# Kernel tuning notes

Measured on AMD Instinct MI355X. Metric: run time of the kernel, lower is better.

Reference implementation:

```python
import jax, jax.numpy as jnp
import numpy as np

B, N, D, H = 8, 2048, 768, 64

def setup_inputs() -> dict:
    key = jax.random.key(0)
    k1, k2, k3, k4 = jax.random.split(key, 4)
    return {
        "input": jax.random.normal(k1, (B, N, D), dtype=jnp.float32),
        "Wq": jax.random.normal(k2, (D, H), dtype=jnp.float32) * (D ** -0.5),
        "Wk": jax.random.normal(k3, (D, H), dtype=jnp.float32) * (D ** -0.5),
        "Wv": jax.random.normal(k4, (D, H), dtype=jnp.float32) * (D ** -0.5),
    }

def reference(input, Wq, Wk, Wv):
    # Projections: [B, N, H]
    Q = jnp.einsum('bnd,dh->bnh', input, Wq)
    K = jnp.einsum('bnd,dh->bnh', input, Wk)
    V = jnp.einsum('bnd,dh->bnh', input, Wv)
    # Raw scores [B, N, N]; mask BEFORE scaling (as in original; -inf/scale == -inf)
    scores = jnp.einsum('bqh,bkh->bqk', Q, K)
    n = input.shape[1]
    causal = jnp.tril(jnp.ones((n, n), dtype=bool))
    scores = jnp.where(causal, scores, -jnp.inf)
    scores = scores / (K.shape[-1] ** 0.5)
    attn = jax.nn.softmax(scores, axis=-1)
    # dropout_rate=0 -> identity (eval mode)
    return jnp.einsum('bqk,bkh->bqh', attn, V)
```

## Files before the change

### kernel.cpp

```cpp
#include <hip/hip_runtime.h>
#include <stdint.h>

typedef __bf16 bf16_t;
typedef __bf16 bf16x8 __attribute__((ext_vector_type(8)));
typedef float floatx4 __attribute__((ext_vector_type(4)));
typedef float floatx16 __attribute__((ext_vector_type(16)));

#define B_ 8
#define N_ 2048
#define D_ 768
#define H_ 64

#define WAIT_VM0()   { __builtin_amdgcn_sched_barrier(0); __builtin_amdgcn_s_waitcnt(0x0F70); __builtin_amdgcn_sched_barrier(0); }
#define WAIT_LGKM0() { __builtin_amdgcn_sched_barrier(0); __builtin_amdgcn_s_waitcnt(0xC07F); __builtin_amdgcn_sched_barrier(0); }

__device__ __forceinline__ bf16_t f2bf(float f) {
    return (bf16_t)f;
}

__device__ __forceinline__ uint32_t pkbf(float lo, float hi_) {
    union { bf16_t b[2]; uint32_t u; } t;
    t.b[0] = (bf16_t)lo; t.b[1] = (bf16_t)hi_;
    return t.u;
}

__device__ __forceinline__ void async_cp16(void* l, const void* g) {
    __builtin_amdgcn_global_load_lds(
        (const __attribute__((address_space(1))) uint32_t*)g,
        (__attribute__((address_space(3))) uint32_t*)l, 16, 0, 0);
}

__global__ void wt_kernel(const float* __restrict__ Wq,
                          const float* __restrict__ Wk,
                          const float* __restrict__ Wv,
                          bf16_t* __restrict__ Wt) {
    const int h = threadIdx.x;
    const int k = blockIdx.x;
    const int s = blockIdx.y;
    const float* W = (s == 0) ? Wq : (s == 1) ? Wk : Wv;
    float v = W[k * H_ + h];
    if (s == 0) v *= 0.125f * 1.4426950408889634f;
    Wt[(size_t)(s * 64 + h) * D_ + k] = f2bf(v);
}

__launch_bounds__(512, 4)
__global__ void proj_kernel(const float* __restrict__ X,
                            const bf16_t* __restrict__ Wt,
                            bf16_t* __restrict__ Qb,
                            bf16_t* __restrict__ Kb,
                            bf16_t* __restrict__ Vt) {
    const int wave = threadIdx.x >> 6;
    const int lane = threadIdx.x & 63;
    const int quad = lane >> 4;
    const int l16  = lane & 15;
    const int rowhalf = wave >> 2;
    const int colq    = wave & 3;
    const int m0blk = blockIdx.x * 32;

    __shared__ __align__(16) float  As[2][32 * 64];
    __shared__ __align__(16) bf16_t Bs[2][192 * 64];

    floatx4 acc[3];
#pragma unroll
    for (int i = 0; i < 3; i++) acc[i] = (floatx4){0.f, 0.f, 0.f, 0.f};

    auto stage = [&](int buf, int k0) {
        {
            const int r = wave * 4 + (lane >> 4);
            const int c = (lane & 15) ^ (r & 15);
            const float* g = X + (size_t)(m0blk + r) * D_ + k0 + c * 4;
            async_cp16((char*)&As[buf][0] + wave * 1024, g);
        }
#pragma unroll
        for (int i = 0; i < 3; i++) {
            const int r = (wave * 3 + i) * 8 + (lane >> 3);
            const int c = (lane & 7) ^ (r & 7);
            const bf16_t* g = Wt + (size_t)r * D_ + k0 + c * 8;
            async_cp16((char*)&Bs[buf][0] + (wave * 3 + i) * 1024, g);
        }
    };

    const int arow = rowhalf * 16 + l16;

    stage(0, 0);
    for (int ch = 0; ch < 12; ch++) {
        __syncthreads();
        if (ch + 1 < 12) stage((ch + 1) & 1, (ch + 1) * 64);

        const char* Ab = (const char*)&As[ch & 1][0];
        const char* Bb = (const char*)&Bs[ch & 1][0];
#pragma unroll
        for (int kh = 0; kh < 2; kh++) {
            const int c0 = kh * 8 + quad * 2;
            float4 xa = *(const float4*)(Ab + arow * 256 + ((c0 ^ l16) & 15) * 16);
            float4 xb = *(const float4*)(Ab + arow * 256 + (((c0 + 1) ^ l16) & 15) * 16);
            bf16x8 af;
            af[0] = f2bf(xa.x); af[1] = f2bf(xa.y);
            af[2] = f2bf(xa.z); af[3] = f2bf(xa.w);
            af[4] = f2bf(xb.x); af[5] = f2bf(xb.y);
            af[6] = f2bf(xb.z); af[7] = f2bf(xb.w);
            const int cb = kh * 4 + quad;
#pragma unroll
            for (int nt = 0; nt < 3; nt++) {
                const int nl = colq * 48 + nt * 16 + l16;
                bf16x8 bf = *(const bf16x8*)(Bb + nl * 128 + ((cb ^ (nl & 7))) * 16);
                acc[nt] = __builtin_amdgcn_mfma_f32_16x16x32_bf16(af, bf, acc[nt], 0, 0, 0);
            }
        }
    }

#pragma unroll
    for (int nt = 0; nt < 3; nt++) {
        const int c = colq * 48 + nt * 16 + l16;
#pragma unroll
        for (int r = 0; r < 4; r++) {
            const int m = m0blk + rowhalf * 16 + quad * 4 + r;
            bf16_t val = f2bf(acc[nt][r]);
            if (c < 64) {
                Qb[(size_t)m * H_ + c] = val;
            } else if (c < 128) {
                Kb[(size_t)m * H_ + (c - 64)] = val;
            } else {
                const int b = m >> 11, n = m & 2047, h = c - 128;
                Vt[((size_t)b * H_ + h) * N_ + n] = val;
            }
        }
    }
}

__launch_bounds__(512, 4)
__global__ void attn_kernel(const bf16_t* __restrict__ Qb,
                            const bf16_t* __restrict__ Kb,
                            const bf16_t* __restrict__ Vt,
                            float* __restrict__ Out) {
    const int x = blockIdx.x;
    const int b = blockIdx.y;
    const int z = blockIdx.z;
    const int qt = z ? (63 - x) : x;
    const int q0 = qt * 32;

    const int tid  = threadIdx.x;
    const int wave = tid >> 6;
    const int lane = tid & 63;
    const int hi   = lane >> 5;
    const int lq   = lane & 31;

    __shared__ __align__(16) char smem[8 * 8192 + 1024];
    char* mybase = smem + wave * 8192;
    float* Ol = (float*)smem;
    float* Ll = (float*)(smem + 65536);

    const bf16_t* KpB = Kb + (size_t)b * N_ * H_;
    const bf16_t* VpB = Vt + (size_t)b * H_ * N_;

    const bf16_t* qrow = Qb + ((size_t)b * N_ + q0 + lq) * H_ + hi * 8;
    bf16x8 qf0 = *(const bf16x8*)(qrow);
    bf16x8 qf1 = *(const bf16x8*)(qrow + 16);
    bf16x8 qf2 = *(const bf16x8*)(qrow + 32);
    bf16x8 qf3 = *(const bf16x8*)(qrow + 48);

    floatx16 o0, o1;
#pragma unroll
    for (int i = 0; i < 16; i++) { o0[i] = 0.f; o1[i] = 0.f; }
    float ls = 0.f;

    const int rK = lane >> 3, cK = lane & 7;
    auto stage_k = [&](int k0, char* buf) {
#pragma unroll
        for (int i = 0; i < 4; i++) {
            const int r = i * 8 + rK;
            const int mk = rK ^ ((i & 1) << 2);
            async_cp16(buf + i * 1024,
                       KpB + (size_t)(k0 + r) * H_ + (cK ^ mk) * 8);
        }
    };

    const int ktm = qt;
    if (wave <= ktm)     stage_k(wave * 32, mybase);
    if (wave + 8 <= ktm) stage_k((wave + 8) * 32, mybase + 4096);

    const int mK = (lq & 7) ^ ((lq & 8) >> 1);

    for (int kt = wave; kt <= ktm; kt += 8) {
        const int k0 = kt * 32;
        char* kb = mybase + (((kt - wave) >> 3) & 1) * 4096;

        if (kt == wave) { WAIT_VM0(); }

        bf16x8 kf0 = *(const bf16x8*)(kb + lq * 128 + (((0 + hi) ^ mK) * 16));
        bf16x8 kf1 = *(const bf16x8*)(kb + lq * 128 + (((2 + hi) ^ mK) * 16));
        bf16x8 kf2 = *(const bf16x8*)(kb + lq * 128 + (((4 + hi) ^ mK) * 16));
        bf16x8 kf3 = *(const bf16x8*)(kb + lq * 128 + (((6 + hi) ^ mK) * 16));
        WAIT_LGKM0();

        const bf16_t* vrow0 = VpB + (size_t)lq * N_ + k0 + 8 * hi;
        const bf16_t* vrow1 = vrow0 + (size_t)32 * N_;
        bf16x8 vf00 = *(const bf16x8*)(vrow0);
        bf16x8 vf01 = *(const bf16x8*)(vrow0 + 16);
        bf16x8 vf10 = *(const bf16x8*)(vrow1);
        bf16x8 vf11 = *(const bf16x8*)(vrow1 + 16);
        __builtin_amdgcn_sched_barrier(0);
        if (kt + 16 <= ktm) stage_k(k0 + 512, kb);

        floatx16 st;
#pragma unroll
        for (int i = 0; i < 16; i++) st[i] = 0.f;
        st = __builtin_amdgcn_mfma_f32_32x32x16_bf16(kf0, qf0, st, 0, 0, 0);
        st = __builtin_amdgcn_mfma_f32_32x32x16_bf16(kf1, qf1, st, 0, 0, 0);
        st = __builtin_amdgcn_mfma_f32_32x32x16_bf16(kf2, qf2, st, 0, 0, 0);
        st = __builtin_amdgcn_mfma_f32_32x32x16_bf16(kf3, qf3, st, 0, 0, 0);

        if (kt < qt) {
#pragma unroll
            for (int r = 0; r < 16; r++) st[r] = exp2f(st[r]);
        } else {
#pragma unroll
            for (int r = 0; r < 16; r++) {
                const int row = (r & 3) + 8 * (r >> 2) + 4 * hi;
                st[r] = (row <= lq) ? exp2f(st[r]) : 0.f;
            }
        }
        {
            float t0 = (st[0] + st[1]) + (st[2] + st[3]);
            float t1 = (st[4] + st[5]) + (st[6] + st[7]);
            float t2 = (st[8] + st[9]) + (st[10] + st[11]);
            float t3 = (st[12] + st[13]) + (st[14] + st[15]);
            ls += (t0 + t1) + (t2 + t3);
        }

        uint32_t pb[8];
#pragma unroll
        for (int t = 0; t < 8; t++) pb[t] = pkbf(st[2 * t], st[2 * t + 1]);
        uint32_t rc[4];
#pragma unroll
        for (int t = 0; t < 4; t++) {
            const uint32_t w = hi ? pb[(t & 1) + 4 * (t >> 1)]
                                  : pb[(t & 1) + 2 + 4 * (t >> 1)];
            rc[t] = (uint32_t)__shfl_xor((int)w, 32, 64);
        }
        union { uint32_t u[4]; bf16x8 v; } f0, f1;
        f0.u[0] = hi ? rc[0] : pb[0]; f0.u[1] = hi ? rc[1] : pb[1];
        f0.u[2] = hi ? pb[2] : rc[0]; f0.u[3] = hi ? pb[3] : rc[1];
        f1.u[0] = hi ? rc[2] : pb[4]; f1.u[1] = hi ? rc[3] : pb[5];
        f1.u[2] = hi ? pb[6] : rc[2]; f1.u[3] = hi ? pb[7] : rc[3];

        o0 = __builtin_amdgcn_mfma_f32_32x32x16_bf16(f0.v, vf00, o0, 0, 0, 0);
        o0 = __builtin_amdgcn_mfma_f32_32x32x16_bf16(f1.v, vf01, o0, 0, 0, 0);
        o1 = __builtin_amdgcn_mfma_f32_32x32x16_bf16(f0.v, vf10, o1, 0, 0, 0);
        o1 = __builtin_amdgcn_mfma_f32_32x32x16_bf16(f1.v, vf11, o1, 0, 0, 0);
    }

    float lst = ls + __shfl_xor(ls, 32, 64);
    __syncthreads();
    if (hi == 0) Ll[wave * 32 + lq] = lst;
#pragma unroll
    for (int r = 0; r < 16; r++) {
        const int q = (r & 3) + 8 * (r >> 2) + 4 * hi;
        Ol[((size_t)wave * 32 + q) * 64 + lq]      = o0[r];
        Ol[((size_t)wave * 32 + q) * 64 + 32 + lq] = o1[r];
    }
    __syncthreads();
    {
        const int q  = tid >> 4;
        const int h4 = (tid & 15) * 4;
        floatx4 a = (floatx4){0.f, 0.f, 0.f, 0.f};
        float l = 0.f;
#pragma unroll
        for (int w = 0; w < 8; w++) {
            const floatx4 part = *(const floatx4*)&Ol[((size_t)w * 32 + q) * 64 + h4];
            a += part;
            l += Ll[w * 32 + q];
        }
        const float inv = 1.0f / l;
        float4 outv = {a[0] * inv, a[1] * inv, a[2] * inv, a[3] * inv};
        *(float4*)&Out[((size_t)b * N_ + q0 + q) * H_ + h4] = outv;
    }
}

extern "C" void kernel_launch(void* const* d_in, const int* in_sizes, int n_in,
                              void* d_out, int out_size, void* d_ws, size_t ws_size,
                              hipStream_t stream) {
    const float* X  = (const float*)d_in[0];
    const float* Wq = (const float*)d_in[1];
    const float* Wk = (const float*)d_in[2];
    const float* Wv = (const float*)d_in[3];
    float* Out = (float*)d_out;

    char* ws = (char*)d_ws;
    bf16_t* Qb = (bf16_t*)(ws);
    bf16_t* Kb = (bf16_t*)(ws + (size_t)(2u << 20));
    bf16_t* Vt = (bf16_t*)(ws + (size_t)(4u << 20));
    bf16_t* Wt = (bf16_t*)(ws + (size_t)(6u << 20));

    hipLaunchKernelGGL(wt_kernel, dim3(768, 3), dim3(64), 0, stream, Wq, Wk, Wv, Wt);
    hipLaunchKernelGGL(proj_kernel, dim3(512), dim3(512), 0, stream, X, Wt, Qb, Kb, Vt);
    hipLaunchKernelGGL(attn_kernel, dim3(32, 8, 2), dim3(512), 0, stream, Qb, Kb, Vt, Out);
}
```

Before: 113.9 us.

## Tile weight transpose via LDS, relax first K wait, use permlane32 swap

The weight-transpose kernel now transposes 64x64 tiles through shared memory with vectorized float4 loads and 16-byte bf16 stores, replacing strided scalar writes. The attention kernel's first wait only drains the first K tile when a second tile is in flight, leaving the prefetch outstanding. The cross-half exchange of probability fragments uses v_permlane32_swap instead of four shuffles plus selects. The wait count assumes exactly four loads per stage, and the swap asm depends on gfx950 support.

```diff
diff --git a/kernel.cpp b/kernel.cpp
--- a/kernel.cpp
+++ b/kernel.cpp
@@ -12,6 +12,7 @@
 #define H_ 64
 
 #define WAIT_VM0()   { __builtin_amdgcn_sched_barrier(0); __builtin_amdgcn_s_waitcnt(0x0F70); __builtin_amdgcn_sched_barrier(0); }
+#define WAIT_VM4()   { __builtin_amdgcn_sched_barrier(0); __builtin_amdgcn_s_waitcnt(0x0F74); __builtin_amdgcn_sched_barrier(0); }
 #define WAIT_LGKM0() { __builtin_amdgcn_sched_barrier(0); __builtin_amdgcn_s_waitcnt(0xC07F); __builtin_amdgcn_sched_barrier(0); }
 
 __device__ __forceinline__ bf16_t f2bf(float f) {
@@ -34,13 +35,34 @@
                           const float* __restrict__ Wk,
                           const float* __restrict__ Wv,
                           bf16_t* __restrict__ Wt) {
-    const int h = threadIdx.x;
-    const int k = blockIdx.x;
-    const int s = blockIdx.y;
+    const int kt = blockIdx.x;
+    const int s  = blockIdx.y;
     const float* W = (s == 0) ? Wq : (s == 1) ? Wk : Wv;
-    float v = W[k * H_ + h];
-    if (s == 0) v *= 0.125f * 1.4426950408889634f;
-    Wt[(size_t)(s * 64 + h) * D_ + k] = f2bf(v);
+    const float scale = (s == 0) ? 0.125f * 1.4426950408889634f : 1.0f;
+
+    __shared__ float T[64][65];
+    const int tid = threadIdx.x;
+    const int r  = tid >> 2;
+    const int cg = tid & 3;
+
+    const float4* src = (const float4*)(W + (size_t)(kt * 64 + r) * H_ + cg * 16);
+#pragma unroll
+    for (int j = 0; j < 4; j++) {
+        float4 v = src[j];
+        T[cg * 16 + j * 4 + 0][r] = v.x;
+        T[cg * 16 + j * 4 + 1][r] = v.y;
+        T[cg * 16 + j * 4 + 2][r] = v.z;
+        T[cg * 16 + j * 4 + 3][r] = v.w;
+    }
+    __syncthreads();
+
+    const int h = r;
+    bf16_t* dst = Wt + (size_t)(s * 64 + h) * D_ + kt * 64 + cg * 16;
+    union { bf16_t b[16]; uint4 q[2]; } o;
+#pragma unroll
+    for (int j = 0; j < 16; j++) o.b[j] = f2bf(T[h][cg * 16 + j] * scale);
+    ((uint4*)dst)[0] = o.q[0];
+    ((uint4*)dst)[1] = o.q[1];
 }
 
 __launch_bounds__(512, 4)
@@ -176,8 +198,9 @@
     };
 
     const int ktm = qt;
-    if (wave <= ktm)     stage_k(wave * 32, mybase);
-    if (wave + 8 <= ktm) stage_k((wave + 8) * 32, mybase + 4096);
+    const bool dbl = (wave + 8 <= ktm);
+    if (wave <= ktm) stage_k(wave * 32, mybase);
+    if (dbl)         stage_k((wave + 8) * 32, mybase + 4096);
 
     const int mK = (lq & 7) ^ ((lq & 8) >> 1);
 
@@ -185,7 +208,10 @@
         const int k0 = kt * 32;
         char* kb = mybase + (((kt - wave) >> 3) & 1) * 4096;
 
-        if (kt == wave) { WAIT_VM0(); }
+        if (kt == wave) {
+            if (dbl) { WAIT_VM4(); }
+            else     { WAIT_VM0(); }
+        }
 
         bf16x8 kf0 = *(const bf16x8*)(kb + lq * 128 + (((0 + hi) ^ mK) * 16));
         bf16x8 kf1 = *(const bf16x8*)(kb + lq * 128 + (((2 + hi) ^ mK) * 16));
@@ -231,18 +257,17 @@
         uint32_t pb[8];
 #pragma unroll
         for (int t = 0; t < 8; t++) pb[t] = pkbf(st[2 * t], st[2 * t + 1]);
-        uint32_t rc[4];
-#pragma unroll
-        for (int t = 0; t < 4; t++) {
-            const uint32_t w = hi ? pb[(t & 1) + 4 * (t >> 1)]
-                                  : pb[(t & 1) + 2 + 4 * (t >> 1)];
-            rc[t] = (uint32_t)__shfl_xor((int)w, 32, 64);
-        }
+        uint32_t a0 = pb[0], b0 = pb[2];
+        uint32_t a1 = pb[1], b1 = pb[3];
+        uint32_t a2 = pb[4], b2 = pb[6];
+        uint32_t a3 = pb[5], b3 = pb[7];
+        asm volatile("v_permlane32_swap_b32 %0, %1" : "+v"(a0), "+v"(b0));
+        asm volatile("v_permlane32_swap_b32 %0, %1" : "+v"(a1), "+v"(b1));
+        asm volatile("v_permlane32_swap_b32 %0, %1" : "+v"(a2), "+v"(b2));
+        asm volatile("v_permlane32_swap_b32 %0, %1" : "+v"(a3), "+v"(b3));
         union { uint32_t u[4]; bf16x8 v; } f0, f1;
-        f0.u[0] = hi ? rc[0] : pb[0]; f0.u[1] = hi ? rc[1] : pb[1];
-        f0.u[2] = hi ? pb[2] : rc[0]; f0.u[3] = hi ? pb[3] : rc[1];
-        f1.u[0] = hi ? rc[2] : pb[4]; f1.u[1] = hi ? rc[3] : pb[5];
-        f1.u[2] = hi ? pb[6] : rc[2]; f1.u[3] = hi ? pb[7] : rc[3];
+        f0.u[0] = a0; f0.u[1] = a1; f0.u[2] = b0; f0.u[3] = b1;
+        f1.u[0] = a2; f1.u[1] = a3; f1.u[2] = b2; f1.u[3] = b3;
 
         o0 = __builtin_amdgcn_mfma_f32_32x32x16_bf16(f0.v, vf00, o0, 0, 0, 0);
         o0 = __builtin_amdgcn_mfma_f32_32x32x16_bf16(f1.v, vf01, o0, 0, 0, 0);
@@ -292,7 +317,7 @@
     bf16_t* Vt = (bf16_t*)(ws + (size_t)(4u << 20));
     bf16_t* Wt = (bf16_t*)(ws + (size_t)(6u << 20));
 
-    hipLaunchKernelGGL(wt_kernel, dim3(768, 3), dim3(64), 0, stream, Wq, Wk, Wv, Wt);
+    hipLaunchKernelGGL(wt_kernel, dim3(12, 3), dim3(256), 0, stream, Wq, Wk, Wv, Wt);
     hipLaunchKernelGGL(proj_kernel, dim3(512), dim3(512), 0, stream, X, Wt, Qb, Kb, Vt);
     hipLaunchKernelGGL(attn_kernel, dim3(32, 8, 2), dim3(512), 0, stream, Qb, Kb, Vt, Out);
 }
```

After: 115.8 us. About the same (+1.7%).
